# Performance work log

Measured on AMD Instinct MI355X. Metric: run time of the kernel, lower is better.

## Reference

```python
import jax, jax.numpy as jnp
import numpy as np

SEQ_LEN = 8192
HIDDEN = 1024
NUM_SPANS = 4096
MAX_W = 32  # max span width (end - start + 1 <= MAX_W)
NEG_INF = -1e9


def setup_inputs() -> dict:
    key = jax.random.key(0)
    k_emb, k_s, k_w, k_aw = jax.random.split(key, 4)
    embeddings = jax.random.normal(k_emb, (1, SEQ_LEN, HIDDEN), dtype=jnp.float32)
    starts = jax.random.randint(k_s, (NUM_SPANS,), 0, SEQ_LEN - MAX_W, dtype=jnp.int32)
    widths = jax.random.randint(k_w, (NUM_SPANS,), 0, MAX_W, dtype=jnp.int32)  # width-1 in [0, MAX_W-1]
    ends = starts + widths
    attn_w = jax.random.normal(k_aw, (HIDDEN,), dtype=jnp.float32) * (HIDDEN ** -0.5)
    attn_b = jnp.zeros((), dtype=jnp.float32)
    return {"embeddings": embeddings, "starts": starts, "ends": ends,
            "attn_w": attn_w, "attn_b": attn_b}


def reference(embeddings, starts, ends, attn_w, attn_b):
    emb = embeddings[0]  # (S_len, H) -- original code indexes batch 0
    # Padded span positions: (num_spans, MAX_W)
    pos = starts[:, None] + jnp.arange(MAX_W, dtype=starts.dtype)[None, :]
    mask = pos <= ends[:, None]
    pos_c = jnp.minimum(pos, SEQ_LEN - 1)
    span_emb = emb[pos_c]  # (num_spans, MAX_W, H) gather
    # Linear(H -> 1) attention scores, masked softmax over span positions
    scores = jnp.einsum("swh,h->sw", span_emb, attn_w) + attn_b
    scores = jnp.where(mask, scores, NEG_INF)
    weights = jax.nn.softmax(scores, axis=1)
    attn_out = jnp.einsum("sw,swh->sh", weights, span_emb)
    start_emb = emb[starts]  # (num_spans, H)
    end_emb = emb[ends]
    return jnp.concatenate([start_emb, end_emb, attn_out], axis=-1)  # (num_spans, 3H)
```

## Files before the change

kernel.cpp:

```cpp
#include <hip/hip_runtime.h>
#include <hip/hip_bf16.h>
#include <math.h>

#define SEQ_LEN  8192
#define HIDDEN   1024
#define NUM_SPANS 4096
#define MAX_W    32
#define NEG_INF  -1e9f

__device__ __forceinline__ float dot4(float4 a, float4 b) {
    return a.x * b.x + a.y * b.y + a.z * b.z + a.w * b.w;
}

__global__ __launch_bounds__(256, 4) void span_repr_kernel(
    const float* __restrict__ emb,
    const int* __restrict__ starts,
    const int* __restrict__ ends,
    const float* __restrict__ attn_w,
    const float* __restrict__ attn_b,
    float* __restrict__ out)
{
    const int s   = blockIdx.x;
    const int tid = threadIdx.x;
    const int w2  = tid >> 6;
    const int c   = tid & 63;

    __shared__ float4 buf[2][4][256];
    __shared__ float  cscore[2][4];

    const int start = starts[s];
    const int end   = ends[s];
    const int wmax  = end - start;
    const float bias = attn_b[0];

    const float4* __restrict__ embr = (const float4*)emb;

    float4 sv = embr[(size_t)start * 256 + tid];
    float4 ev = embr[(size_t)end   * 256 + tid];

    const float4* __restrict__ wv4 = (const float4*)attn_w;
    const float4 wv0 = wv4[c];
    const float4 wv1 = wv4[c + 64];
    const float4 wv2 = wv4[c + 128];
    const float4 wv3 = wv4[c + 192];

    const int nc = (wmax >> 2) + 1;

    {
        const int r  = w2;
        const int rc = min(r, wmax);
        const float4* __restrict__ row = embr + (size_t)(start + rc) * 256;
        float4 r0 = row[c];
        float4 r1 = row[c + 64];
        float4 r2 = row[c + 128];
        float4 r3 = row[c + 192];
        float p = dot4(r0, wv0) + dot4(r1, wv1) + dot4(r2, wv2) + dot4(r3, wv3);
        #pragma unroll
        for (int off = 32; off > 0; off >>= 1)
            p += __shfl_xor(p, off, 64);
        if (c == 0) cscore[0][w2] = (r <= wmax) ? (p + bias) : NEG_INF;
        buf[0][w2][c]       = r0;
        buf[0][w2][c + 64]  = r1;
        buf[0][w2][c + 128] = r2;
        buf[0][w2][c + 192] = r3;
    }

    float4* __restrict__ out4 = (float4*)(out + (size_t)s * (3 * HIDDEN));
    out4[tid]       = sv;
    out4[256 + tid] = ev;

    __syncthreads();

    float4 acc = make_float4(0.f, 0.f, 0.f, 0.f);
    float m = -INFINITY;
    float l = 0.0f;

    for (int ck = 0; ck < nc; ++ck) {
        const int par = ck & 1;
        const int pn  = par ^ 1;
        const bool more = (ck + 1 < nc);

        float4 r0, r1, r2, r3;
        if (more) {
            const int r  = (ck + 1) * 4 + w2;
            const int rc = min(r, wmax);
            const float4* __restrict__ row = embr + (size_t)(start + rc) * 256;
            r0 = row[c];
            r1 = row[c + 64];
            r2 = row[c + 128];
            r3 = row[c + 192];
            __builtin_amdgcn_sched_barrier(0);
        }

        const float s0 = cscore[par][0];
        const float s1 = cscore[par][1];
        const float s2 = cscore[par][2];
        const float s3 = cscore[par][3];
        const float cm = fmaxf(fmaxf(s0, s1), fmaxf(s2, s3));
        const float mn = fmaxf(m, cm);
        const float alpha = __expf(m - mn);
        const float e0 = __expf(s0 - mn);
        const float e1 = __expf(s1 - mn);
        const float e2 = __expf(s2 - mn);
        const float e3 = __expf(s3 - mn);
        l = l * alpha + (e0 + e1 + e2 + e3);

        const float4 b0 = buf[par][0][tid];
        const float4 b1 = buf[par][1][tid];
        const float4 b2 = buf[par][2][tid];
        const float4 b3 = buf[par][3][tid];
        acc.x = acc.x * alpha + e0 * b0.x + e1 * b1.x + e2 * b2.x + e3 * b3.x;
        acc.y = acc.y * alpha + e0 * b0.y + e1 * b1.y + e2 * b2.y + e3 * b3.y;
        acc.z = acc.z * alpha + e0 * b0.z + e1 * b1.z + e2 * b2.z + e3 * b3.z;
        acc.w = acc.w * alpha + e0 * b0.w + e1 * b1.w + e2 * b2.w + e3 * b3.w;
        m = mn;

        if (more) {
            float p = dot4(r0, wv0) + dot4(r1, wv1) + dot4(r2, wv2) + dot4(r3, wv3);
            #pragma unroll
            for (int off = 32; off > 0; off >>= 1)
                p += __shfl_xor(p, off, 64);
            const int r = (ck + 1) * 4 + w2;
            if (c == 0) cscore[pn][w2] = (r <= wmax) ? (p + bias) : NEG_INF;
            buf[pn][w2][c]       = r0;
            buf[pn][w2][c + 64]  = r1;
            buf[pn][w2][c + 128] = r2;
            buf[pn][w2][c + 192] = r3;
        }
        __syncthreads();
    }

    const float inv = 1.0f / l;
    out4[512 + tid] = make_float4(acc.x * inv, acc.y * inv,
                                  acc.z * inv, acc.w * inv);
}

extern "C" void kernel_launch(void* const* d_in, const int* in_sizes, int n_in,
                              void* d_out, int out_size, void* d_ws, size_t ws_size,
                              hipStream_t stream) {
    const float* emb    = (const float*)d_in[0];
    const int*   starts = (const int*)d_in[1];
    const int*   ends   = (const int*)d_in[2];
    const float* attn_w = (const float*)d_in[3];
    const float* attn_b = (const float*)d_in[4];
    float* out = (float*)d_out;

    span_repr_kernel<<<NUM_SPANS, 256, 0, stream>>>(emb, starts, ends, attn_w, attn_b, out);
}
```

Baseline: 125.0 us.

## Assign one wavefront per span with register-resident online softmax

Work is remapped so each 64-lane wavefront handles a whole span, iterating rows serially with a one-row register prefetch. This removes the shared-memory double buffers and the block-wide barriers of the old 4-rows-per-chunk scheme. The start and end rows are taken from the first and last loaded rows instead of separate loads. Outputs use nontemporal stores. The tradeoff is serialized per-row latency within a wave, with load imbalance across the variable span widths and no cross-wave overlap inside a span.

```diff
diff --git a/kernel.cpp b/kernel.cpp
--- a/kernel.cpp
+++ b/kernel.cpp
@@ -1,15 +1,20 @@
 #include <hip/hip_runtime.h>
-#include <hip/hip_bf16.h>
 #include <math.h>
 
-#define SEQ_LEN  8192
-#define HIDDEN   1024
+#define SEQ_LEN   8192
+#define HIDDEN    1024
 #define NUM_SPANS 4096
-#define MAX_W    32
-#define NEG_INF  -1e9f
+#define MAX_W     32
+
+typedef float f4v __attribute__((ext_vector_type(4)));
 
 __device__ __forceinline__ float dot4(float4 a, float4 b) {
     return a.x * b.x + a.y * b.y + a.z * b.z + a.w * b.w;
+}
+
+__device__ __forceinline__ void nt_store4(float4* p, float4 v) {
+    f4v x = { v.x, v.y, v.z, v.w };
+    __builtin_nontemporal_store(x, (f4v*)p);
 }
 
 __global__ __launch_bounds__(256, 4) void span_repr_kernel(
@@ -20,23 +25,16 @@
     const float* __restrict__ attn_b,
     float* __restrict__ out)
 {
-    const int s   = blockIdx.x;
     const int tid = threadIdx.x;
     const int w2  = tid >> 6;
     const int c   = tid & 63;
-
-    __shared__ float4 buf[2][4][256];
-    __shared__ float  cscore[2][4];
+    const int s   = (blockIdx.x << 2) + w2;
 
     const int start = starts[s];
-    const int end   = ends[s];
-    const int wmax  = end - start;
+    const int wmax  = ends[s] - start;
     const float bias = attn_b[0];
 
-    const float4* __restrict__ embr = (const float4*)emb;
-
-    float4 sv = embr[(size_t)start * 256 + tid];
-    float4 ev = embr[(size_t)end   * 256 + tid];
+    const float4* __restrict__ embr = (const float4*)emb + (size_t)start * 256;
 
     const float4* __restrict__ wv4 = (const float4*)attn_w;
     const float4 wv0 = wv4[c];
@@ -44,95 +42,72 @@
     const float4 wv2 = wv4[c + 128];
     const float4 wv3 = wv4[c + 192];
 
-    const int nc = (wmax >> 2) + 1;
+    float4* __restrict__ out4 = (float4*)(out + (size_t)s * (3 * HIDDEN));
 
-    {
-        const int r  = w2;
-        const int rc = min(r, wmax);
-        const float4* __restrict__ row = embr + (size_t)(start + rc) * 256;
-        float4 r0 = row[c];
-        float4 r1 = row[c + 64];
-        float4 r2 = row[c + 128];
-        float4 r3 = row[c + 192];
-        float p = dot4(r0, wv0) + dot4(r1, wv1) + dot4(r2, wv2) + dot4(r3, wv3);
+    float4 v0 = embr[c];
+    float4 v1 = embr[c + 64];
+    float4 v2 = embr[c + 128];
+    float4 v3 = embr[c + 192];
+
+    nt_store4(&out4[c],       v0);
+    nt_store4(&out4[c + 64],  v1);
+    nt_store4(&out4[c + 128], v2);
+    nt_store4(&out4[c + 192], v3);
+
+    float4 a0 = make_float4(0.f, 0.f, 0.f, 0.f);
+    float4 a1 = make_float4(0.f, 0.f, 0.f, 0.f);
+    float4 a2 = make_float4(0.f, 0.f, 0.f, 0.f);
+    float4 a3 = make_float4(0.f, 0.f, 0.f, 0.f);
+    float m = -INFINITY;
+    float l = 0.0f;
+
+    for (int r = 0; r <= wmax; ++r) {
+        const float4* __restrict__ nr = embr + (size_t)min(r + 1, wmax) * 256;
+        float4 n0 = nr[c];
+        float4 n1 = nr[c + 64];
+        float4 n2 = nr[c + 128];
+        float4 n3 = nr[c + 192];
+        __builtin_amdgcn_sched_barrier(0);
+
+        float p = dot4(v0, wv0) + dot4(v1, wv1) + dot4(v2, wv2) + dot4(v3, wv3);
         #pragma unroll
         for (int off = 32; off > 0; off >>= 1)
             p += __shfl_xor(p, off, 64);
-        if (c == 0) cscore[0][w2] = (r <= wmax) ? (p + bias) : NEG_INF;
-        buf[0][w2][c]       = r0;
-        buf[0][w2][c + 64]  = r1;
-        buf[0][w2][c + 128] = r2;
-        buf[0][w2][c + 192] = r3;
+        const float sc = p + bias;
+
+        if (sc > m) {
+            const float alpha = __expf(m - sc);
+            a0.x *= alpha; a0.y *= alpha; a0.z *= alpha; a0.w *= alpha;
+            a1.x *= alpha; a1.y *= alpha; a1.z *= alpha; a1.w *= alpha;
+            a2.x *= alpha; a2.y *= alpha; a2.z *= alpha; a2.w *= alpha;
+            a3.x *= alpha; a3.y *= alpha; a3.z *= alpha; a3.w *= alpha;
+            l *= alpha;
+            m = sc;
+        }
+        const float e = __expf(sc - m);
+        l += e;
+        a0.x += e * v0.x; a0.y += e * v0.y; a0.z += e * v0.z; a0.w += e * v0.w;
+        a1.x += e * v1.x; a1.y += e * v1.y; a1.z += e * v1.z; a1.w += e * v1.w;
+        a2.x += e * v2.x; a2.y += e * v2.y; a2.z += e * v2.z; a2.w += e * v2.w;
+        a3.x += e * v3.x; a3.y += e * v3.y; a3.z += e * v3.z; a3.w += e * v3.w;
+
+        v0 = n0; v1 = n1; v2 = n2; v3 = n3;
     }
 
-    float4* __restrict__ out4 = (float4*)(out + (size_t)s * (3 * HIDDEN));
-    out4[tid]       = sv;
-    out4[256 + tid] = ev;
-
-    __syncthreads();
-
-    float4 acc = make_float4(0.f, 0.f, 0.f, 0.f);
-    float m = -INFINITY;
-    float l = 0.0f;
-
-    for (int ck = 0; ck < nc; ++ck) {
-        const int par = ck & 1;
-        const int pn  = par ^ 1;
-        const bool more = (ck + 1 < nc);
-
-        float4 r0, r1, r2, r3;
-        if (more) {
-            const int r  = (ck + 1) * 4 + w2;
-            const int rc = min(r, wmax);
-            const float4* __restrict__ row = embr + (size_t)(start + rc) * 256;
-            r0 = row[c];
-            r1 = row[c + 64];
-            r2 = row[c + 128];
-            r3 = row[c + 192];
-            __builtin_amdgcn_sched_barrier(0);
-        }
-
-        const float s0 = cscore[par][0];
-        const float s1 = cscore[par][1];
-        const float s2 = cscore[par][2];
-        const float s3 = cscore[par][3];
-        const float cm = fmaxf(fmaxf(s0, s1), fmaxf(s2, s3));
-        const float mn = fmaxf(m, cm);
-        const float alpha = __expf(m - mn);
-        const float e0 = __expf(s0 - mn);
-        const float e1 = __expf(s1 - mn);
-        const float e2 = __expf(s2 - mn);
-        const float e3 = __expf(s3 - mn);
-        l = l * alpha + (e0 + e1 + e2 + e3);
-
-        const float4 b0 = buf[par][0][tid];
-        const float4 b1 = buf[par][1][tid];
-        const float4 b2 = buf[par][2][tid];
-        const float4 b3 = buf[par][3][tid];
-        acc.x = acc.x * alpha + e0 * b0.x + e1 * b1.x + e2 * b2.x + e3 * b3.x;
-        acc.y = acc.y * alpha + e0 * b0.y + e1 * b1.y + e2 * b2.y + e3 * b3.y;
-        acc.z = acc.z * alpha + e0 * b0.z + e1 * b1.z + e2 * b2.z + e3 * b3.z;
-        acc.w = acc.w * alpha + e0 * b0.w + e1 * b1.w + e2 * b2.w + e3 * b3.w;
-        m = mn;
-
-        if (more) {
-            float p = dot4(r0, wv0) + dot4(r1, wv1) + dot4(r2, wv2) + dot4(r3, wv3);
-            #pragma unroll
-            for (int off = 32; off > 0; off >>= 1)
-                p += __shfl_xor(p, off, 64);
-            const int r = (ck + 1) * 4 + w2;
-            if (c == 0) cscore[pn][w2] = (r <= wmax) ? (p + bias) : NEG_INF;
-            buf[pn][w2][c]       = r0;
-            buf[pn][w2][c + 64]  = r1;
-            buf[pn][w2][c + 128] = r2;
-            buf[pn][w2][c + 192] = r3;
-        }
-        __syncthreads();
-    }
+    nt_store4(&out4[256 + c],       v0);
+    nt_store4(&out4[256 + c + 64],  v1);
+    nt_store4(&out4[256 + c + 128], v2);
+    nt_store4(&out4[256 + c + 192], v3);
 
     const float inv = 1.0f / l;
-    out4[512 + tid] = make_float4(acc.x * inv, acc.y * inv,
-                                  acc.z * inv, acc.w * inv);
+    nt_store4(&out4[512 + c],
+              make_float4(a0.x * inv, a0.y * inv, a0.z * inv, a0.w * inv));
+    nt_store4(&out4[512 + c + 64],
+              make_float4(a1.x * inv, a1.y * inv, a1.z * inv, a1.w * inv));
+    nt_store4(&out4[512 + c + 128],
+              make_float4(a2.x * inv, a2.y * inv, a2.z * inv, a2.w * inv));
+    nt_store4(&out4[512 + c + 192],
+              make_float4(a3.x * inv, a3.y * inv, a3.z * inv, a3.w * inv));
 }
 
 extern "C" void kernel_launch(void* const* d_in, const int* in_sizes, int n_in,
@@ -145,5 +120,5 @@
     const float* attn_b = (const float*)d_in[4];
     float* out = (float*)d_out;
 
-    span_repr_kernel<<<NUM_SPANS, 256, 0, stream>>>(emb, starts, ends, attn_w, attn_b, out);
+    span_repr_kernel<<<NUM_SPANS / 4, 256, 0, stream>>>(emb, starts, ends, attn_w, attn_b, out);
 }
```

Measured after the change: 124.2 us. About the same (-0.7%).
